# Performance work log

Hardware: AMD Instinct MI355X
Metric: run time of the kernel (lower is better)

## Reference

```python
import jax, jax.numpy as jnp
import numpy as np


def _conv1d_same(seq, w, b):
    # seq: (N, 1, C), w: (1, 1, K) odd K, bias (1,). SAME padding, stride 1.
    k = w.shape[-1]
    p = (k - 1) // 2
    out = jax.lax.conv_general_dilated(
        seq, w, window_strides=(1,), padding=[(p, p)],
        dimension_numbers=("NCH", "OIH", "NCH"))
    return out + b[None, :, None]


def setup_inputs() -> dict:
    key = jax.random.key(0)
    k1, k2, k3 = jax.random.split(key, 3)
    N, C, H, W = 32, 512, 32, 32
    x = jax.random.normal(k1, (N, C, H, W), dtype=jnp.float32)
    wq = jax.random.normal(k2, (1, 1, 5), dtype=jnp.float32) * 0.2
    bq = jax.random.normal(k3, (1,), dtype=jnp.float32) * 0.1
    return {"x": x, "wq": wq, "bq": bq}


def reference(x, wq, bq):
    N, C, H, W = x.shape
    # Global average pool over spatial dims -> (N, 1, C)
    gap = jnp.mean(x, axis=(2, 3)).reshape(N, 1, C)
    # NOTE: original module applies conv_q to BOTH query and key (conv_k unused)
    query = jax.nn.sigmoid(_conv1d_same(gap, wq, bq))          # (N, 1, C)
    key_t = jnp.transpose(query, (0, 2, 1))                    # (N, C, 1)
    # Outer product key @ query -> (N, C, C), softmax over flattened C*C
    qk = jnp.einsum("nci,nij->ncj", key_t, query)              # (N, C, C)
    qk = jax.nn.softmax(qk.reshape(N, C * C), axis=-1).reshape(N, C, C)
    # value: (N, H*W, C)
    value = jnp.transpose(x, (0, 2, 3, 1)).reshape(N, H * W, C)
    att = jnp.einsum("npc,ncd->npd", value, qk)                # (N, HW, C)
    att = jnp.transpose(att, (0, 2, 1)).reshape(N, C, H, W)
    return x * att
```

## Files before the change

### kernel.cpp

```cpp
#include <hip/hip_runtime.h>
#include <math.h>

#define NB 32
#define CC 512
#define HW 1024
#define NJ 10
#define DG 8

__device__ __forceinline__ float wave_reduce(float s) {
#pragma unroll
  for (int off = 32; off; off >>= 1) s += __shfl_down(s, off, 64);
  return s;
}

__global__ void k_gap(const float* __restrict__ x, float* __restrict__ gap) {
  int b = blockIdx.x;
  const float4* xp = (const float4*)(x + (size_t)b * HW);
  float4 v = xp[threadIdx.x];
  float s = v.x + v.y + v.z + v.w;
  s = wave_reduce(s);
  __shared__ float red[4];
  int lane = threadIdx.x & 63, wv = threadIdx.x >> 6;
  if (lane == 0) red[wv] = s;
  __syncthreads();
  if (threadIdx.x == 0)
    gap[b] = (red[0] + red[1] + red[2] + red[3]) * (1.0f / 1024.0f);
}

__global__ void k_qz(const float* __restrict__ gap, const float* __restrict__ wq,
                     const float* __restrict__ bq, float* __restrict__ q,
                     float* __restrict__ invZ) {
  int n = blockIdx.x, c = threadIdx.x;
  const float* g = gap + n * CC;
  float z = bq[0];
#pragma unroll
  for (int j = 0; j < 5; ++j) {
    int idx = c + j - 2;
    float gv = (idx >= 0 && idx < CC) ? g[idx] : 0.0f;
    z = fmaf(gv, wq[j], z);
  }
  float qv = 1.0f / (1.0f + expf(-z));
  q[n * CC + c] = qv;
  float acc[NJ];
  {
    float w = 1.0f;
#pragma unroll
    for (int j = 0; j < NJ; ++j) { acc[j] = w; w *= qv; }
  }
#pragma unroll
  for (int j = 0; j < NJ; ++j) acc[j] = wave_reduce(acc[j]);
  __shared__ float red[NJ][8];
  int lane = c & 63, wv = c >> 6;
  if (lane == 0) {
#pragma unroll
    for (int j = 0; j < NJ; ++j) red[j][wv] = acc[j];
  }
  __syncthreads();
  if (c == 0) {
    const float cj[NJ] = {1.f, 1.f, 0.5f, 1.f / 6.f, 1.f / 24.f, 1.f / 120.f,
                          1.f / 720.f, 1.f / 5040.f, 1.f / 40320.f, 1.f / 362880.f};
    float Zv = 0.0f;
#pragma unroll
    for (int j = 0; j < NJ; ++j) {
      float P = 0.0f;
#pragma unroll
      for (int w8 = 0; w8 < 8; ++w8) P += red[j][w8];
      Zv = fmaf(cj[j] * P, P, Zv);
    }
    invZ[n] = 1.0f / Zv;
  }
}

__global__ void k_sj(const float* __restrict__ x, const float* __restrict__ q,
                     float* __restrict__ sp, int nchunk, int cs) {
  int b = blockIdx.x;
  int n = b / nchunk, ch = b - n * nchunk;
  int c0 = ch * cs;
  __shared__ float qs[CC];
  for (int i = threadIdx.x; i < cs; i += blockDim.x) qs[i] = q[n * CC + c0 + i];
  __syncthreads();
  float4 acc[NJ];
#pragma unroll
  for (int j = 0; j < NJ; ++j) acc[j] = make_float4(0.f, 0.f, 0.f, 0.f);
  const float4* xp = (const float4*)x + (size_t)(n * CC + c0) * (HW / 4) + threadIdx.x;
  for (int ci = 0; ci < cs; ++ci) {
    float4 xv = xp[(size_t)ci * (HW / 4)];
    float qc = qs[ci];
    float w = 1.0f;
#pragma unroll
    for (int j = 0; j < NJ; ++j) {
      acc[j].x = fmaf(w, xv.x, acc[j].x);
      acc[j].y = fmaf(w, xv.y, acc[j].y);
      acc[j].z = fmaf(w, xv.z, acc[j].z);
      acc[j].w = fmaf(w, xv.w, acc[j].w);
      w *= qc;
    }
  }
  float4* spp = (float4*)sp + (size_t)b * NJ * (HW / 4) + threadIdx.x;
#pragma unroll
  for (int j = 0; j < NJ; ++j) spp[j * (HW / 4)] = acc[j];
}

__global__ void k_red(const float* __restrict__ sp, float* __restrict__ s, int nchunk) {
  int b = blockIdx.x;
  int n = b / NJ, j = b - n * NJ;
  float4 a = make_float4(0.f, 0.f, 0.f, 0.f);
  const float4* spp = (const float4*)sp;
  for (int ch = 0; ch < nchunk; ++ch) {
    float4 v = spp[((size_t)(n * nchunk + ch) * NJ + j) * (HW / 4) + threadIdx.x];
    a.x += v.x; a.y += v.y; a.z += v.z; a.w += v.w;
  }
  ((float4*)s)[(size_t)b * (HW / 4) + threadIdx.x] = a;
}

__global__ void k_out(const float* __restrict__ x, const float* __restrict__ q,
                      const float* __restrict__ s, const float* __restrict__ invZ,
                      float* __restrict__ out) {
  int b = blockIdx.x;
  int n = b / (CC / DG), dg = b - n * (CC / DG);
  int d0 = dg * DG;
  int t = threadIdx.x;
  const float4* s4 = (const float4*)s + (size_t)n * NJ * (HW / 4) + t;
  float4 sj[NJ];
#pragma unroll
  for (int j = 0; j < NJ; ++j) sj[j] = s4[j * (HW / 4)];
  float iz = invZ[n];
  const float cj[NJ] = {1.f, 1.f, 0.5f, 1.f / 6.f, 1.f / 24.f, 1.f / 120.f,
                        1.f / 720.f, 1.f / 5040.f, 1.f / 40320.f, 1.f / 362880.f};
#pragma unroll
  for (int di = 0; di < DG; ++di) {
    float qd = q[n * CC + d0 + di];
    float w = iz;
    float4 att = make_float4(0.f, 0.f, 0.f, 0.f);
#pragma unroll
    for (int j = 0; j < NJ; ++j) {
      float a = cj[j] * w;
      att.x = fmaf(a, sj[j].x, att.x);
      att.y = fmaf(a, sj[j].y, att.y);
      att.z = fmaf(a, sj[j].z, att.z);
      att.w = fmaf(a, sj[j].w, att.w);
      w *= qd;
    }
    size_t idx = (size_t)(n * CC + d0 + di) * (HW / 4) + t;
    float4 xv = ((const float4*)x)[idx];
    float4 o;
    o.x = xv.x * att.x; o.y = xv.y * att.y;
    o.z = xv.z * att.z; o.w = xv.w * att.w;
    ((float4*)out)[idx] = o;
  }
}

extern "C" void kernel_launch(void* const* d_in, const int* in_sizes, int n_in,
                              void* d_out, int out_size, void* d_ws, size_t ws_size,
                              hipStream_t stream) {
  const float* x  = (const float*)d_in[0];
  const float* wq = (const float*)d_in[1];
  const float* bq = (const float*)d_in[2];
  float* out = (float*)d_out;
  char* ws = (char*)d_ws;

  float* gap  = (float*)(ws);
  float* q    = (float*)(ws + 65536);
  float* invZ = (float*)(ws + 131072);
  float* s    = (float*)(ws + 131584);
  size_t base = 131584 + (size_t)NB * NJ * HW * 4;
  float* sp   = (float*)(ws + base);

  int nchunk = 16;
  while (nchunk > 1 && base + (size_t)nchunk * NB * NJ * HW * 4 > ws_size) nchunk >>= 1;
  int cs = CC / nchunk;
  bool skip_red = false;
  if (base + (size_t)nchunk * NB * NJ * HW * 4 > ws_size) {
    sp = s; skip_red = true;
  }
  if (nchunk == 1) { sp = s; skip_red = true; }

  k_gap<<<NB * CC, 256, 0, stream>>>(x, gap);
  k_qz<<<NB, CC, 0, stream>>>(gap, wq, bq, q, invZ);
  k_sj<<<NB * nchunk, 256, 0, stream>>>(x, q, sp, nchunk, cs);
  if (!skip_red) k_red<<<NB * NJ, 256, 0, stream>>>(sp, s, nchunk);
  k_out<<<NB * (CC / DG), 256, 0, stream>>>(x, q, s, invZ, out);
}
```

Measured before the change: 148.6 us.

## Fuse q/Z, power-sum and output stages into one register-resident kernel

Collapses the q/invZ, partial power-sum, reduction and output kernels into a single kernel. Each block owns a 64-pixel slice for one batch across all 512 channels and keeps its x values in registers, so x is read from global memory once for the sums and the output instead of twice, and the sp/s workspace round-trips disappear. The gap kernel now has each wave reduce four rows, using fewer blocks. In exchange every block recomputes the conv/sigmoid/Z for its batch, and it needs heavy register use (16 float4 of x plus 10 float4 accumulators) and 512 blocks of 512 threads, which may limit occupancy.

Result: faster. 131.3 us (-11.7%).

```diff
diff --git a/kernel.cpp b/kernel.cpp
--- a/kernel.cpp
+++ b/kernel.cpp
@@ -5,7 +5,6 @@
 #define CC 512
 #define HW 1024
 #define NJ 10
-#define DG 8
 
 __device__ __forceinline__ float wave_reduce(float s) {
 #pragma unroll
@@ -13,140 +12,155 @@
   return s;
 }
 
-__global__ void k_gap(const float* __restrict__ x, float* __restrict__ gap) {
-  int b = blockIdx.x;
-  const float4* xp = (const float4*)(x + (size_t)b * HW);
-  float4 v = xp[threadIdx.x];
-  float s = v.x + v.y + v.z + v.w;
-  s = wave_reduce(s);
-  __shared__ float red[4];
-  int lane = threadIdx.x & 63, wv = threadIdx.x >> 6;
-  if (lane == 0) red[wv] = s;
-  __syncthreads();
-  if (threadIdx.x == 0)
-    gap[b] = (red[0] + red[1] + red[2] + red[3]) * (1.0f / 1024.0f);
-}
-
-__global__ void k_qz(const float* __restrict__ gap, const float* __restrict__ wq,
-                     const float* __restrict__ bq, float* __restrict__ q,
-                     float* __restrict__ invZ) {
-  int n = blockIdx.x, c = threadIdx.x;
-  const float* g = gap + n * CC;
-  float z = bq[0];
+__global__ __launch_bounds__(256) void k_gap(const float* __restrict__ x,
+                                             float* __restrict__ gap) {
+  int wv = threadIdx.x >> 6, lane = threadIdx.x & 63;
+  int r0 = blockIdx.x * 16;
 #pragma unroll
-  for (int j = 0; j < 5; ++j) {
-    int idx = c + j - 2;
-    float gv = (idx >= 0 && idx < CC) ? g[idx] : 0.0f;
-    z = fmaf(gv, wq[j], z);
-  }
-  float qv = 1.0f / (1.0f + expf(-z));
-  q[n * CC + c] = qv;
-  float acc[NJ];
-  {
-    float w = 1.0f;
+  for (int it = 0; it < 4; ++it) {
+    int row = r0 + wv * 4 + it;
+    const float4* xp = (const float4*)x + (size_t)row * 256;
+    float s = 0.f;
 #pragma unroll
-    for (int j = 0; j < NJ; ++j) { acc[j] = w; w *= qv; }
-  }
-#pragma unroll
-  for (int j = 0; j < NJ; ++j) acc[j] = wave_reduce(acc[j]);
-  __shared__ float red[NJ][8];
-  int lane = c & 63, wv = c >> 6;
-  if (lane == 0) {
-#pragma unroll
-    for (int j = 0; j < NJ; ++j) red[j][wv] = acc[j];
-  }
-  __syncthreads();
-  if (c == 0) {
-    const float cj[NJ] = {1.f, 1.f, 0.5f, 1.f / 6.f, 1.f / 24.f, 1.f / 120.f,
-                          1.f / 720.f, 1.f / 5040.f, 1.f / 40320.f, 1.f / 362880.f};
-    float Zv = 0.0f;
-#pragma unroll
-    for (int j = 0; j < NJ; ++j) {
-      float P = 0.0f;
-#pragma unroll
-      for (int w8 = 0; w8 < 8; ++w8) P += red[j][w8];
-      Zv = fmaf(cj[j] * P, P, Zv);
+    for (int k = 0; k < 4; ++k) {
+      float4 v = xp[lane + 64 * k];
+      s += v.x + v.y + v.z + v.w;
     }
-    invZ[n] = 1.0f / Zv;
+    s = wave_reduce(s);
+    if (lane == 0) gap[row] = s * (1.0f / 1024.0f);
   }
 }
 
-__global__ void k_sj(const float* __restrict__ x, const float* __restrict__ q,
-                     float* __restrict__ sp, int nchunk, int cs) {
-  int b = blockIdx.x;
-  int n = b / nchunk, ch = b - n * nchunk;
-  int c0 = ch * cs;
+__global__ __launch_bounds__(512) void k_fused(const float* __restrict__ x,
+                                               const float* __restrict__ gap,
+                                               const float* __restrict__ wq,
+                                               const float* __restrict__ bq,
+                                               float* __restrict__ out) {
+  int n = blockIdx.x >> 4, pblk = blockIdx.x & 15;
+  int t = threadIdx.x;
+  int cg = t >> 4, pg = t & 15;
+  int wv = t >> 6, lane = t & 63;
+
   __shared__ float qs[CC];
-  for (int i = threadIdx.x; i < cs; i += blockDim.x) qs[i] = q[n * CC + c0 + i];
+  __shared__ float wred[8][NJ];
+  __shared__ float4 sred[8][16][NJ + 1];
+  __shared__ float4 sfin[16][NJ + 1];
+  __shared__ float invZ_sh;
+
+  const float cj[NJ] = {1.f, 1.f, 0.5f, 1.f / 6.f, 1.f / 24.f, 1.f / 120.f,
+                        1.f / 720.f, 1.f / 5040.f, 1.f / 40320.f, 1.f / 362880.f};
+
+  float4 xv[16];
+  const float4* x4 = (const float4*)x;
+  size_t base = (size_t)(n * CC + cg * 16) * 256 + (size_t)pblk * 16 + pg;
+#pragma unroll
+  for (int i = 0; i < 16; ++i) xv[i] = x4[base + (size_t)i * 256];
+
+  {
+    int c = t;
+    const float* g = gap + n * CC;
+    float z = bq[0];
+#pragma unroll
+    for (int k = 0; k < 5; ++k) {
+      int idx = c + k - 2;
+      float gv = (idx >= 0 && idx < CC) ? g[idx] : 0.f;
+      z = fmaf(gv, wq[k], z);
+    }
+    float qv = 1.f / (1.f + expf(-z));
+    qs[c] = qv;
+    float pj[NJ];
+    float pw = 1.f;
+#pragma unroll
+    for (int j = 0; j < NJ; ++j) { pj[j] = pw; pw *= qv; }
+#pragma unroll
+    for (int j = 0; j < NJ; ++j) pj[j] = wave_reduce(pj[j]);
+    if (lane == 0) {
+#pragma unroll
+      for (int j = 0; j < NJ; ++j) wred[wv][j] = pj[j];
+    }
+  }
   __syncthreads();
+  if (t == 0) {
+    float Z = 0.f;
+#pragma unroll
+    for (int j = 0; j < NJ; ++j) {
+      float P = 0.f;
+#pragma unroll
+      for (int w8 = 0; w8 < 8; ++w8) P += wred[w8][j];
+      Z = fmaf(cj[j] * P, P, Z);
+    }
+    invZ_sh = 1.f / Z;
+  }
+
   float4 acc[NJ];
 #pragma unroll
   for (int j = 0; j < NJ; ++j) acc[j] = make_float4(0.f, 0.f, 0.f, 0.f);
-  const float4* xp = (const float4*)x + (size_t)(n * CC + c0) * (HW / 4) + threadIdx.x;
-  for (int ci = 0; ci < cs; ++ci) {
-    float4 xv = xp[(size_t)ci * (HW / 4)];
-    float qc = qs[ci];
-    float w = 1.0f;
+#pragma unroll
+  for (int i = 0; i < 16; ++i) {
+    float qc = qs[cg * 16 + i];
+    float4 v = xv[i];
+    float w = 1.f;
 #pragma unroll
     for (int j = 0; j < NJ; ++j) {
-      acc[j].x = fmaf(w, xv.x, acc[j].x);
-      acc[j].y = fmaf(w, xv.y, acc[j].y);
-      acc[j].z = fmaf(w, xv.z, acc[j].z);
-      acc[j].w = fmaf(w, xv.w, acc[j].w);
+      acc[j].x = fmaf(w, v.x, acc[j].x);
+      acc[j].y = fmaf(w, v.y, acc[j].y);
+      acc[j].z = fmaf(w, v.z, acc[j].z);
+      acc[j].w = fmaf(w, v.w, acc[j].w);
       w *= qc;
     }
   }
-  float4* spp = (float4*)sp + (size_t)b * NJ * (HW / 4) + threadIdx.x;
 #pragma unroll
-  for (int j = 0; j < NJ; ++j) spp[j * (HW / 4)] = acc[j];
-}
+  for (int j = 0; j < NJ; ++j) {
+    acc[j].x += __shfl_xor(acc[j].x, 16, 64);
+    acc[j].y += __shfl_xor(acc[j].y, 16, 64);
+    acc[j].z += __shfl_xor(acc[j].z, 16, 64);
+    acc[j].w += __shfl_xor(acc[j].w, 16, 64);
+    acc[j].x += __shfl_xor(acc[j].x, 32, 64);
+    acc[j].y += __shfl_xor(acc[j].y, 32, 64);
+    acc[j].z += __shfl_xor(acc[j].z, 32, 64);
+    acc[j].w += __shfl_xor(acc[j].w, 32, 64);
+  }
+  if (lane < 16) {
+#pragma unroll
+    for (int j = 0; j < NJ; ++j) sred[wv][lane][j] = acc[j];
+  }
+  __syncthreads();
+  if (t < 160) {
+    int pp = t / NJ, j = t - pp * NJ;
+    float4 a = make_float4(0.f, 0.f, 0.f, 0.f);
+#pragma unroll
+    for (int w8 = 0; w8 < 8; ++w8) {
+      float4 v = sred[w8][pp][j];
+      a.x += v.x; a.y += v.y; a.z += v.z; a.w += v.w;
+    }
+    float sc = cj[j] * invZ_sh;
+    a.x *= sc; a.y *= sc; a.z *= sc; a.w *= sc;
+    sfin[pp][j] = a;
+  }
+  __syncthreads();
 
-__global__ void k_red(const float* __restrict__ sp, float* __restrict__ s, int nchunk) {
-  int b = blockIdx.x;
-  int n = b / NJ, j = b - n * NJ;
-  float4 a = make_float4(0.f, 0.f, 0.f, 0.f);
-  const float4* spp = (const float4*)sp;
-  for (int ch = 0; ch < nchunk; ++ch) {
-    float4 v = spp[((size_t)(n * nchunk + ch) * NJ + j) * (HW / 4) + threadIdx.x];
-    a.x += v.x; a.y += v.y; a.z += v.z; a.w += v.w;
-  }
-  ((float4*)s)[(size_t)b * (HW / 4) + threadIdx.x] = a;
-}
-
-__global__ void k_out(const float* __restrict__ x, const float* __restrict__ q,
-                      const float* __restrict__ s, const float* __restrict__ invZ,
-                      float* __restrict__ out) {
-  int b = blockIdx.x;
-  int n = b / (CC / DG), dg = b - n * (CC / DG);
-  int d0 = dg * DG;
-  int t = threadIdx.x;
-  const float4* s4 = (const float4*)s + (size_t)n * NJ * (HW / 4) + t;
   float4 sj[NJ];
 #pragma unroll
-  for (int j = 0; j < NJ; ++j) sj[j] = s4[j * (HW / 4)];
-  float iz = invZ[n];
-  const float cj[NJ] = {1.f, 1.f, 0.5f, 1.f / 6.f, 1.f / 24.f, 1.f / 120.f,
-                        1.f / 720.f, 1.f / 5040.f, 1.f / 40320.f, 1.f / 362880.f};
+  for (int j = 0; j < NJ; ++j) sj[j] = sfin[pg][j];
+  float4* o4 = (float4*)out;
 #pragma unroll
-  for (int di = 0; di < DG; ++di) {
-    float qd = q[n * CC + d0 + di];
-    float w = iz;
+  for (int i = 0; i < 16; ++i) {
+    float qd = qs[cg * 16 + i];
+    float w = 1.f;
     float4 att = make_float4(0.f, 0.f, 0.f, 0.f);
 #pragma unroll
     for (int j = 0; j < NJ; ++j) {
-      float a = cj[j] * w;
-      att.x = fmaf(a, sj[j].x, att.x);
-      att.y = fmaf(a, sj[j].y, att.y);
-      att.z = fmaf(a, sj[j].z, att.z);
-      att.w = fmaf(a, sj[j].w, att.w);
+      att.x = fmaf(w, sj[j].x, att.x);
+      att.y = fmaf(w, sj[j].y, att.y);
+      att.z = fmaf(w, sj[j].z, att.z);
+      att.w = fmaf(w, sj[j].w, att.w);
       w *= qd;
     }
-    size_t idx = (size_t)(n * CC + d0 + di) * (HW / 4) + t;
-    float4 xv = ((const float4*)x)[idx];
+    float4 xvv = xv[i];
     float4 o;
-    o.x = xv.x * att.x; o.y = xv.y * att.y;
-    o.z = xv.z * att.z; o.w = xv.w * att.w;
-    ((float4*)out)[idx] = o;
+    o.x = xvv.x * att.x; o.y = xvv.y * att.y;
+    o.z = xvv.z * att.z; o.w = xvv.w * att.w;
+    o4[base + (size_t)i * 256] = o;
   }
 }
 
@@ -157,27 +171,8 @@
   const float* wq = (const float*)d_in[1];
   const float* bq = (const float*)d_in[2];
   float* out = (float*)d_out;
-  char* ws = (char*)d_ws;
+  float* gap = (float*)d_ws;
 
-  float* gap  = (float*)(ws);
-  float* q    = (float*)(ws + 65536);
-  float* invZ = (float*)(ws + 131072);
-  float* s    = (float*)(ws + 131584);
-  size_t base = 131584 + (size_t)NB * NJ * HW * 4;
-  float* sp   = (float*)(ws + base);
-
-  int nchunk = 16;
-  while (nchunk > 1 && base + (size_t)nchunk * NB * NJ * HW * 4 > ws_size) nchunk >>= 1;
-  int cs = CC / nchunk;
-  bool skip_red = false;
-  if (base + (size_t)nchunk * NB * NJ * HW * 4 > ws_size) {
-    sp = s; skip_red = true;
-  }
-  if (nchunk == 1) { sp = s; skip_red = true; }
-
-  k_gap<<<NB * CC, 256, 0, stream>>>(x, gap);
-  k_qz<<<NB, CC, 0, stream>>>(gap, wq, bq, q, invZ);
-  k_sj<<<NB * nchunk, 256, 0, stream>>>(x, q, sp, nchunk, cs);
-  if (!skip_red) k_red<<<NB * NJ, 256, 0, stream>>>(sp, s, nchunk);
-  k_out<<<NB * (CC / DG), 256, 0, stream>>>(x, q, s, invZ, out);
+  k_gap<<<NB * CC / 16, 256, 0, stream>>>(x, gap);
+  k_fused<<<NB * 16, 512, 0, stream>>>(x, gap, wq, bq, out);
 }
```
